# Kernel optimization log

Measured on AMD Instinct MI355X. Metric: run time of the kernel, lower is better.

Reference implementation:

```python
import jax, jax.numpy as jnp
import numpy as np

B, S, D, H = 8, 1024, 1024, 16
DK = D // H  # 64


def setup_inputs() -> dict:
    key = jax.random.key(0)
    k1, k2, k3, k4, k5, k6 = jax.random.split(key, 6)
    mask = jax.random.randint(k1, (B, S, S), 0, 2, dtype=jnp.int32)
    x_key_value = jax.random.normal(k2, (B, S, D), dtype=jnp.float32)
    # per-head projection weights (stacked over heads)
    scale = 1.0 / np.sqrt(D)
    wq = jax.random.normal(k3, (H, D, DK), dtype=jnp.float32) * scale
    wk = jax.random.normal(k4, (H, D, DK), dtype=jnp.float32) * scale
    wv = jax.random.normal(k5, (H, D, DK), dtype=jnp.float32) * scale
    # output projection (nn.Parameter; randomized here for a meaningful baseline)
    wo = jax.random.normal(k6, (D, D), dtype=jnp.float32) * scale
    return {"mask": mask, "x_key_value": x_key_value, "wq": wq, "wk": wk, "wv": wv, "wo": wo}


def reference(mask, x_key_value, wq, wk, wv, wo):
    # batched multi-head SDPA (equivalent to the per-head Python loop + concat)
    q = jnp.einsum('bsd,hdk->bhsk', x_key_value, wq)
    k = jnp.einsum('btd,hdk->bhtk', x_key_value, wk)
    v = jnp.einsum('btd,hdk->bhtk', x_key_value, wv)
    scores = jnp.einsum('bhsk,bhtk->bhst', q, k) / jnp.sqrt(jnp.asarray(DK, q.dtype))
    scores = jnp.where(mask[:, None, :, :] != 0, scores, jnp.asarray(-1e9, q.dtype))
    attn = jax.nn.softmax(scores, axis=-1)
    ctx = jnp.einsum('bhst,bhtk->bhsk', attn, v)
    # concat heads along feature dim: [B,S,H*DK]
    ctx = ctx.transpose(0, 2, 1, 3).reshape(B, S, D)
    # output proj (dropout is identity in eval) + residual
    res = ctx @ wo + x_key_value
    # torch.layer_norm over normalized_shape = (S, D), no affine, eps=1e-5
    mean = jnp.mean(res, axis=(1, 2), keepdims=True)
    var = jnp.var(res, axis=(1, 2), keepdims=True)
    return (res - mean) / jnp.sqrt(var + 1e-5)
```

## Files before the change

### kernel.cpp

```cpp
#include <hip/hip_runtime.h>

typedef unsigned short u16;
typedef __attribute__((ext_vector_type(8))) short bf16x8;
typedef __attribute__((ext_vector_type(4))) float f32x4;


static __device__ __forceinline__ u16 f2bf(float f) {
    union { float f; unsigned u; } v; v.f = f;
    unsigned r = v.u + 0x7fffu + ((v.u >> 16) & 1u);
    return (u16)(r >> 16);
}

static __device__ __forceinline__ f32x4 mfma16(bf16x8 a, bf16x8 b, f32x4 c) {
    return __builtin_amdgcn_mfma_f32_16x16x32_bf16(a, b, c, 0, 0, 0);
}

static __device__ __forceinline__ void load_lds16(const u16* g, u16* l) {
    __builtin_amdgcn_global_load_lds((const __attribute__((address_space(1))) unsigned*)(const void*)g,
                                     (__attribute__((address_space(3))) unsigned*)(void*)l, 16, 0, 0);
}

__global__ __launch_bounds__(256) void cvt_x_kernel(const float* __restrict__ x, u16* __restrict__ xb) {
    int i = (blockIdx.x * 256 + threadIdx.x) * 4;
    float4 v = *(const float4*)(x + i);
    ushort4 o;
    o.x = f2bf(v.x); o.y = f2bf(v.y); o.z = f2bf(v.z); o.w = f2bf(v.w);
    *(ushort4*)(xb + i) = o;
}

__global__ __launch_bounds__(256) void cvt_w_kernel(const float* __restrict__ wq, const float* __restrict__ wk,
                                                    const float* __restrict__ wv, const float* __restrict__ wo,
                                                    u16* __restrict__ wt, u16* __restrict__ wot) {
    int o = blockIdx.x * 256 + threadIdx.x;
    if (o < 3145728) {
        int z = o >> 20;
        int rem = o & 1048575;
        int n = rem >> 10;
        int d = rem & 1023;
        int h = n >> 6, kk = n & 63;
        const float* w = (z == 0) ? wq : (z == 1) ? wk : wv;
        wt[o] = f2bf(w[h * 65536 + d * 64 + kk]);
    } else {
        int oo = o - 3145728;
        int n = oo >> 10, d = oo & 1023;
        wot[oo] = f2bf(wo[d * 1024 + n]);
    }
}

__global__ __launch_bounds__(256) void pack_mask_kernel(const int* __restrict__ mask, uint2* __restrict__ mb) {
    long long wi = (long long)blockIdx.x * 4 + (threadIdx.x >> 6);
    int lane = threadIdx.x & 63;
    int v = mask[wi * 64 + lane];
    unsigned long long bal = __ballot(v != 0);
    if (lane == 0) {
        uint2 o; o.x = (unsigned)bal; o.y = (unsigned)(bal >> 32);
        mb[wi] = o;
    }
}

__global__ __launch_bounds__(256) void qkv_gemm_kernel(const u16* __restrict__ xb, const u16* __restrict__ wt,
                                                       u16* __restrict__ qb, u16* __restrict__ kb,
                                                       u16* __restrict__ vtb) {
    __shared__ __align__(16) u16 As[128 * 64];
    __shared__ __align__(16) u16 Bs[128 * 64];

    int t = threadIdx.x;
    int lane = t & 63, w = t >> 6;
    int wm = w & 1, wn = w >> 1;
    int l16 = lane & 15, quad = lane >> 4;
    int sw = l16 & 7;

    int m0 = blockIdx.x * 128;
    int n0g = blockIdx.y * 128;

    int srow = t >> 3;
    int skp = ((t & 7) ^ (srow & 7)) * 8;
    const u16* ga0 = xb + (m0 + srow) * 1024 + skp;
    const u16* gb0 = wt + (n0g + srow) * 1024 + skp;

    int arow0 = wm * 64 + l16;
    int brow0 = wn * 64 + l16;

    f32x4 acc[4][4];
#pragma unroll
    for (int i = 0; i < 4; ++i)
#pragma unroll
        for (int j = 0; j < 4; ++j) acc[i][j] = (f32x4){0.f, 0.f, 0.f, 0.f};

    for (int kb0 = 0; kb0 < 1024; kb0 += 64) {
        __syncthreads();
#pragma unroll
        for (int c = 0; c < 4; ++c)
            load_lds16(ga0 + c * 32768 + kb0, &As[c * 2048 + t * 8]);
#pragma unroll
        for (int c = 0; c < 4; ++c)
            load_lds16(gb0 + c * 32768 + kb0, &Bs[c * 2048 + t * 8]);
        __syncthreads();

#pragma unroll
        for (int kh = 0; kh < 2; ++kh) {
            int kidx = ((kh << 2) + quad) ^ sw;
            bf16x8 af[4], bfr[4];
#pragma unroll
            for (int i = 0; i < 4; ++i)
                af[i] = *(const bf16x8*)&As[(arow0 + i * 16) * 64 + kidx * 8];
#pragma unroll
            for (int j = 0; j < 4; ++j)
                bfr[j] = *(const bf16x8*)&Bs[(brow0 + j * 16) * 64 + kidx * 8];
#pragma unroll
            for (int i = 0; i < 4; ++i)
#pragma unroll
                for (int j = 0; j < 4; ++j)
                    acc[i][j] = mfma16(af[i], bfr[j], acc[i][j]);
        }
    }

    int z = blockIdx.y >> 3;
    float qscale = (z == 0) ? 0.125f : 1.0f;
#pragma unroll
    for (int j = 0; j < 4; ++j) {
        int ng = n0g + wn * 64 + j * 16 + l16;
        int nl = ng & 1023;
        int h = nl >> 6, kk = nl & 63;
#pragma unroll
        for (int i = 0; i < 4; ++i) {
#pragma unroll
            for (int r = 0; r < 4; ++r) {
                int m = m0 + wm * 64 + i * 16 + quad * 4 + r;
                int b_ = m >> 10, s = m & 1023;
                u16 val = f2bf(acc[i][j][r] * qscale);
                if (z == 0)      qb[((b_ * 16 + h) * 1024 + s) * 64 + kk] = val;
                else if (z == 1) kb[((b_ * 16 + h) * 1024 + s) * 64 + kk] = val;
                else             vtb[((b_ * 16 + h) * 64 + kk) * 1024 + s] = val;
            }
        }
    }
}

__global__ __launch_bounds__(256) void attn_kernel(const u16* __restrict__ qb, const u16* __restrict__ kb,
                                                   const u16* __restrict__ vtb, const uint2* __restrict__ mb,
                                                   u16* __restrict__ ctx) {
    __shared__ __align__(16) u16 Ks[64 * 64];
    __shared__ __align__(16) u16 Vs[64 * 64];
    __shared__ __align__(16) u16 P[4][16][72];

    int t = threadIdx.x;
    int w = t >> 6, lane = t & 63;
    int l16 = lane & 15, quad = lane >> 4;
    int h = blockIdx.y, b = blockIdx.z;
    int q0 = blockIdx.x * 64 + w * 16;

    const u16* Q = qb + (b * 16 + h) * 65536;
    const u16* K = kb + (b * 16 + h) * 65536;
    const u16* Vt = vtb + (b * 16 + h) * 65536;
    const uint2* MB = mb + (b * 1024 + q0) * 16;

    int srow = t >> 3;
    int skp = ((t & 7) ^ (srow & 7)) * 8;
    const u16* gk0 = K + srow * 64 + skp;
    const u16* gv0 = Vt + srow * 1024 + skp;

    bf16x8 qf0 = *(const bf16x8*)(Q + (q0 + l16) * 64 + quad * 8);
    bf16x8 qf1 = *(const bf16x8*)(Q + (q0 + l16) * 64 + 32 + quad * 8);

    f32x4 O[4];
#pragma unroll
    for (int j = 0; j < 4; ++j) O[j] = (f32x4){0.f, 0.f, 0.f, 0.f};
    float lsum[4] = {0.f, 0.f, 0.f, 0.f};

    int sw = l16 & 7;

    for (int kt0 = 0; kt0 < 16; ++kt0) {
        int k0 = kt0 * 64;
        __syncthreads();
#pragma unroll
        for (int c = 0; c < 2; ++c) {
            load_lds16(gk0 + (k0 + c * 32) * 64, &Ks[c * 2048 + t * 8]);
            load_lds16(gv0 + c * 32 * 1024 + k0, &Vs[c * 2048 + t * 8]);
        }
        __syncthreads();

        f32x4 s[4];
#pragma unroll
        for (int kt = 0; kt < 4; ++kt) {
            int row = kt * 16 + l16;
            bf16x8 klo = *(const bf16x8*)&Ks[row * 64 + ((quad ^ sw) * 8)];
            bf16x8 khi = *(const bf16x8*)&Ks[row * 64 + (((4 + quad) ^ sw) * 8)];
            f32x4 z = {0.f, 0.f, 0.f, 0.f};
            z = mfma16(qf0, klo, z);
            z = mfma16(qf1, khi, z);
            s[kt] = z;
        }

#pragma unroll
        for (int r = 0; r < 4; ++r) {
            int qrow = quad * 4 + r;
            uint2 mw = MB[qrow * 16 + kt0];
#pragma unroll
            for (int kt = 0; kt < 4; ++kt) {
                unsigned wsel = (kt < 2) ? mw.x : mw.y;
                unsigned bit = (wsel >> ((kt & 1) * 16 + l16)) & 1u;
                float e = bit ? __expf(s[kt][r]) : 0.f;
                lsum[r] += e;
                P[w][qrow][kt * 16 + l16] = f2bf(e);
            }
        }

        bf16x8 pf0 = *(const bf16x8*)&P[w][l16][quad * 8];
        bf16x8 pf1 = *(const bf16x8*)&P[w][l16][32 + quad * 8];

#pragma unroll
        for (int j = 0; j < 4; ++j) {
            int row = j * 16 + l16;
            bf16x8 vlo = *(const bf16x8*)&Vs[row * 64 + ((quad ^ sw) * 8)];
            bf16x8 vhi = *(const bf16x8*)&Vs[row * 64 + (((4 + quad) ^ sw) * 8)];
            O[j] = mfma16(pf0, vlo, O[j]);
            O[j] = mfma16(pf1, vhi, O[j]);
        }
    }

#pragma unroll
    for (int r = 0; r < 4; ++r) {
        float s = lsum[r];
        s += __shfl_xor(s, 1);
        s += __shfl_xor(s, 2);
        s += __shfl_xor(s, 4);
        s += __shfl_xor(s, 8);
        lsum[r] = s;
    }

#pragma unroll
    for (int r = 0; r < 4; ++r) {
        int sI = q0 + quad * 4 + r;
        float inv = 1.0f / lsum[r];
        int base = (b * 1024 + sI) * 1024 + h * 64;
#pragma unroll
        for (int j = 0; j < 4; ++j)
            ctx[base + j * 16 + l16] = f2bf(O[j][r] * inv);
    }
}

__global__ __launch_bounds__(256) void oproj_gemm_kernel(const u16* __restrict__ ctxb, const u16* __restrict__ wot,
                                                         const float* __restrict__ x, float* __restrict__ res) {
    __shared__ __align__(16) u16 As[128 * 64];
    __shared__ __align__(16) u16 Bs[128 * 64];

    int t = threadIdx.x;
    int lane = t & 63, w = t >> 6;
    int wm = w & 1, wn = w >> 1;
    int l16 = lane & 15, quad = lane >> 4;
    int sw = l16 & 7;

    int m0 = blockIdx.x * 128;
    int n0 = blockIdx.y * 128;

    int srow = t >> 3;
    int skp = ((t & 7) ^ (srow & 7)) * 8;
    const u16* ga0 = ctxb + (m0 + srow) * 1024 + skp;
    const u16* gb0 = wot + (n0 + srow) * 1024 + skp;

    int arow0 = wm * 64 + l16;
    int brow0 = wn * 64 + l16;

    f32x4 acc[4][4];
#pragma unroll
    for (int i = 0; i < 4; ++i)
#pragma unroll
        for (int j = 0; j < 4; ++j) acc[i][j] = (f32x4){0.f, 0.f, 0.f, 0.f};

    for (int kb0 = 0; kb0 < 1024; kb0 += 64) {
        __syncthreads();
#pragma unroll
        for (int c = 0; c < 4; ++c)
            load_lds16(ga0 + c * 32768 + kb0, &As[c * 2048 + t * 8]);
#pragma unroll
        for (int c = 0; c < 4; ++c)
            load_lds16(gb0 + c * 32768 + kb0, &Bs[c * 2048 + t * 8]);
        __syncthreads();

#pragma unroll
        for (int kh = 0; kh < 2; ++kh) {
            int kidx = ((kh << 2) + quad) ^ sw;
            bf16x8 af[4], bfr[4];
#pragma unroll
            for (int i = 0; i < 4; ++i)
                af[i] = *(const bf16x8*)&As[(arow0 + i * 16) * 64 + kidx * 8];
#pragma unroll
            for (int j = 0; j < 4; ++j)
                bfr[j] = *(const bf16x8*)&Bs[(brow0 + j * 16) * 64 + kidx * 8];
#pragma unroll
            for (int i = 0; i < 4; ++i)
#pragma unroll
                for (int j = 0; j < 4; ++j)
                    acc[i][j] = mfma16(af[i], bfr[j], acc[i][j]);
        }
    }

#pragma unroll
    for (int i = 0; i < 4; ++i) {
#pragma unroll
        for (int r = 0; r < 4; ++r) {
            int m = m0 + wm * 64 + i * 16 + quad * 4 + r;
#pragma unroll
            for (int j = 0; j < 4; ++j) {
                int n = n0 + wn * 64 + j * 16 + l16;
                res[m * 1024 + n] = acc[i][j][r] + x[m * 1024 + n];
            }
        }
    }
}

__global__ __launch_bounds__(256) void reduce_kernel(const float* __restrict__ res, float* __restrict__ sums) {
    int b = blockIdx.y;
    const float* p = res + b * 1048576;
    float s = 0.f, s2 = 0.f;
    for (int i = blockIdx.x * 256 + threadIdx.x; i < 1048576; i += 16384) {
        float v = p[i];
        s += v; s2 += v * v;
    }
#pragma unroll
    for (int off = 32; off > 0; off >>= 1) {
        s += __shfl_down(s, off);
        s2 += __shfl_down(s2, off);
    }
    __shared__ float ls[4], ls2[4];
    int w = threadIdx.x >> 6, lane = threadIdx.x & 63;
    if (lane == 0) { ls[w] = s; ls2[w] = s2; }
    __syncthreads();
    if (threadIdx.x == 0) {
        atomicAdd(&sums[b * 2 + 0], ls[0] + ls[1] + ls[2] + ls[3]);
        atomicAdd(&sums[b * 2 + 1], ls2[0] + ls2[1] + ls2[2] + ls2[3]);
    }
}

__global__ __launch_bounds__(256) void norm_kernel(const float* __restrict__ res, const float* __restrict__ sums,
                                                   float* __restrict__ out) {
    int i = blockIdx.x * 256 + threadIdx.x;
    int b = i >> 20;
    float mean = sums[b * 2 + 0] * (1.0f / 1048576.0f);
    float var = sums[b * 2 + 1] * (1.0f / 1048576.0f) - mean * mean;
    float rs = rsqrtf(var + 1e-5f);
    out[i] = (res[i] - mean) * rs;
}


extern "C" void kernel_launch(void* const* d_in, const int* in_sizes, int n_in,
                              void* d_out, int out_size, void* d_ws, size_t ws_size,
                              hipStream_t stream) {
    const int* mask  = (const int*)d_in[0];
    const float* x   = (const float*)d_in[1];
    const float* wq  = (const float*)d_in[2];
    const float* wk  = (const float*)d_in[3];
    const float* wv  = (const float*)d_in[4];
    const float* wo  = (const float*)d_in[5];
    float* out = (float*)d_out;

    char* ws = (char*)d_ws;
    u16* xb    = (u16*)(ws + 0);
    u16* wt    = (u16*)(ws + 16777216);
    u16* wot   = (u16*)(ws + 23068672);
    u16* qb    = (u16*)(ws + 25165824);
    u16* kb    = (u16*)(ws + 41943040);
    u16* vtb   = (u16*)(ws + 58720256);
    float* res = (float*)(ws + 25165824);
    float* sums = (float*)(ws + 75497472);
    uint2* mbits = (uint2*)(ws + 76546048);
    u16* ctxb  = (u16*)d_out;

    hipMemsetAsync(sums, 0, 64, stream);
    pack_mask_kernel<<<32768, 256, 0, stream>>>(mask, mbits);
    cvt_x_kernel<<<8192, 256, 0, stream>>>(x, xb);
    cvt_w_kernel<<<16384, 256, 0, stream>>>(wq, wk, wv, wo, wt, wot);
    qkv_gemm_kernel<<<dim3(64, 24), 256, 0, stream>>>(xb, wt, qb, kb, vtb);
    attn_kernel<<<dim3(16, 16, 8), 256, 0, stream>>>(qb, kb, vtb, mbits, ctxb);
    oproj_gemm_kernel<<<dim3(64, 8), 256, 0, stream>>>(ctxb, wot, x, res);
    reduce_kernel<<<dim3(64, 8), 256, 0, stream>>>(res, sums);
    norm_kernel<<<32768, 256, 0, stream>>>(res, sums, out);
}
```

Measured before the change: 361.9 us.

## Merge prep kernels, fuse LayerNorm stats into o-proj epilogue, prefetch mask words

The three preprocessing kernels (x conversion, weight transpose-convert, mask bit-packing) are merged into one launch that dispatches on block index. The separate reduction kernel is removed: the output-projection epilogue now accumulates per-block sum and sum-of-squares and atomically adds them per batch, which avoids re-reading the full residual tensor. In the attention loop the mask words are loaded before the barrier so their latency overlaps the K/V tile loads. The cost is more atomics per batch and extra register pressure in the GEMM epilogue.

```diff
diff --git a/kernel.cpp b/kernel.cpp
--- a/kernel.cpp
+++ b/kernel.cpp
@@ -20,41 +20,43 @@
                                      (__attribute__((address_space(3))) unsigned*)(void*)l, 16, 0, 0);
 }
 
-__global__ __launch_bounds__(256) void cvt_x_kernel(const float* __restrict__ x, u16* __restrict__ xb) {
-    int i = (blockIdx.x * 256 + threadIdx.x) * 4;
-    float4 v = *(const float4*)(x + i);
-    ushort4 o;
-    o.x = f2bf(v.x); o.y = f2bf(v.y); o.z = f2bf(v.z); o.w = f2bf(v.w);
-    *(ushort4*)(xb + i) = o;
-}
-
-__global__ __launch_bounds__(256) void cvt_w_kernel(const float* __restrict__ wq, const float* __restrict__ wk,
-                                                    const float* __restrict__ wv, const float* __restrict__ wo,
-                                                    u16* __restrict__ wt, u16* __restrict__ wot) {
-    int o = blockIdx.x * 256 + threadIdx.x;
-    if (o < 3145728) {
-        int z = o >> 20;
-        int rem = o & 1048575;
-        int n = rem >> 10;
-        int d = rem & 1023;
-        int h = n >> 6, kk = n & 63;
-        const float* w = (z == 0) ? wq : (z == 1) ? wk : wv;
-        wt[o] = f2bf(w[h * 65536 + d * 64 + kk]);
+__global__ __launch_bounds__(256) void prep_kernel(const float* __restrict__ x,
+                                                   const float* __restrict__ wq, const float* __restrict__ wk,
+                                                   const float* __restrict__ wv, const float* __restrict__ wo,
+                                                   const int* __restrict__ mask,
+                                                   u16* __restrict__ xb, u16* __restrict__ wt,
+                                                   u16* __restrict__ wot, uint2* __restrict__ mb) {
+    int bid = blockIdx.x;
+    if (bid < 8192) {
+        int i = (bid * 256 + threadIdx.x) * 4;
+        float4 v = *(const float4*)(x + i);
+        ushort4 o;
+        o.x = f2bf(v.x); o.y = f2bf(v.y); o.z = f2bf(v.z); o.w = f2bf(v.w);
+        *(ushort4*)(xb + i) = o;
+    } else if (bid < 24576) {
+        int o = (bid - 8192) * 256 + threadIdx.x;
+        if (o < 3145728) {
+            int z = o >> 20;
+            int rem = o & 1048575;
+            int n = rem >> 10;
+            int d = rem & 1023;
+            int h = n >> 6, kk = n & 63;
+            const float* w = (z == 0) ? wq : (z == 1) ? wk : wv;
+            wt[o] = f2bf(w[h * 65536 + d * 64 + kk]);
+        } else {
+            int oo = o - 3145728;
+            int n = oo >> 10, d = oo & 1023;
+            wot[oo] = f2bf(wo[d * 1024 + n]);
+        }
     } else {
-        int oo = o - 3145728;
-        int n = oo >> 10, d = oo & 1023;
-        wot[oo] = f2bf(wo[d * 1024 + n]);
-    }
-}
-
-__global__ __launch_bounds__(256) void pack_mask_kernel(const int* __restrict__ mask, uint2* __restrict__ mb) {
-    long long wi = (long long)blockIdx.x * 4 + (threadIdx.x >> 6);
-    int lane = threadIdx.x & 63;
-    int v = mask[wi * 64 + lane];
-    unsigned long long bal = __ballot(v != 0);
-    if (lane == 0) {
-        uint2 o; o.x = (unsigned)bal; o.y = (unsigned)(bal >> 32);
-        mb[wi] = o;
+        long long wi = (long long)(bid - 24576) * 4 + (threadIdx.x >> 6);
+        int lane = threadIdx.x & 63;
+        int v = mask[wi * 64 + lane];
+        unsigned long long bal = __ballot(v != 0);
+        if (lane == 0) {
+            uint2 o; o.x = (unsigned)bal; o.y = (unsigned)(bal >> 32);
+            mb[wi] = o;
+        }
     }
 }
 
@@ -172,6 +174,12 @@
 
     for (int kt0 = 0; kt0 < 16; ++kt0) {
         int k0 = kt0 * 64;
+
+        uint2 mw[4];
+#pragma unroll
+        for (int r = 0; r < 4; ++r)
+            mw[r] = MB[(quad * 4 + r) * 16 + kt0];
+
         __syncthreads();
 #pragma unroll
         for (int c = 0; c < 2; ++c) {
@@ -195,10 +203,9 @@
 #pragma unroll
         for (int r = 0; r < 4; ++r) {
             int qrow = quad * 4 + r;
-            uint2 mw = MB[qrow * 16 + kt0];
 #pragma unroll
             for (int kt = 0; kt < 4; ++kt) {
-                unsigned wsel = (kt < 2) ? mw.x : mw.y;
+                unsigned wsel = (kt < 2) ? mw[r].x : mw[r].y;
                 unsigned bit = (wsel >> ((kt & 1) * 16 + l16)) & 1u;
                 float e = bit ? __expf(s[kt][r]) : 0.f;
                 lsum[r] += e;
@@ -241,7 +248,8 @@
 }
 
 __global__ __launch_bounds__(256) void oproj_gemm_kernel(const u16* __restrict__ ctxb, const u16* __restrict__ wot,
-                                                         const float* __restrict__ x, float* __restrict__ res) {
+                                                         const float* __restrict__ x, float* __restrict__ res,
+                                                         float* __restrict__ sums) {
     __shared__ __align__(16) u16 As[128 * 64];
     __shared__ __align__(16) u16 Bs[128 * 64];
 
@@ -296,6 +304,7 @@
         }
     }
 
+    float ps = 0.f, ps2 = 0.f;
 #pragma unroll
     for (int i = 0; i < 4; ++i) {
 #pragma unroll
@@ -304,30 +313,23 @@
 #pragma unroll
             for (int j = 0; j < 4; ++j) {
                 int n = n0 + wn * 64 + j * 16 + l16;
-                res[m * 1024 + n] = acc[i][j][r] + x[m * 1024 + n];
+                float v = acc[i][j][r] + x[m * 1024 + n];
+                res[m * 1024 + n] = v;
+                ps += v; ps2 += v * v;
             }
         }
     }
-}
-
-__global__ __launch_bounds__(256) void reduce_kernel(const float* __restrict__ res, float* __restrict__ sums) {
-    int b = blockIdx.y;
-    const float* p = res + b * 1048576;
-    float s = 0.f, s2 = 0.f;
-    for (int i = blockIdx.x * 256 + threadIdx.x; i < 1048576; i += 16384) {
-        float v = p[i];
-        s += v; s2 += v * v;
-    }
+
 #pragma unroll
     for (int off = 32; off > 0; off >>= 1) {
-        s += __shfl_down(s, off);
-        s2 += __shfl_down(s2, off);
+        ps += __shfl_xor(ps, off);
+        ps2 += __shfl_xor(ps2, off);
     }
     __shared__ float ls[4], ls2[4];
-    int w = threadIdx.x >> 6, lane = threadIdx.x & 63;
-    if (lane == 0) { ls[w] = s; ls2[w] = s2; }
+    if (lane == 0) { ls[w] = ps; ls2[w] = ps2; }
     __syncthreads();
-    if (threadIdx.x == 0) {
+    if (t == 0) {
+        int b = blockIdx.x >> 3;
         atomicAdd(&sums[b * 2 + 0], ls[0] + ls[1] + ls[2] + ls[3]);
         atomicAdd(&sums[b * 2 + 1], ls2[0] + ls2[1] + ls2[2] + ls2[3]);
     }
@@ -368,12 +370,9 @@
     u16* ctxb  = (u16*)d_out;
 
     hipMemsetAsync(sums, 0, 64, stream);
-    pack_mask_kernel<<<32768, 256, 0, stream>>>(mask, mbits);
-    cvt_x_kernel<<<8192, 256, 0, stream>>>(x, xb);
-    cvt_w_kernel<<<16384, 256, 0, stream>>>(wq, wk, wv, wo, wt, wot);
+    prep_kernel<<<57344, 256, 0, stream>>>(x, wq, wk, wv, wo, mask, xb, wt, wot, mbits);
     qkv_gemm_kernel<<<dim3(64, 24), 256, 0, stream>>>(xb, wt, qb, kb, vtb);
     attn_kernel<<<dim3(16, 16, 8), 256, 0, stream>>>(qb, kb, vtb, mbits, ctxb);
-    oproj_gemm_kernel<<<dim3(64, 8), 256, 0, stream>>>(ctxb, wot, x, res);
-    reduce_kernel<<<dim3(64, 8), 256, 0, stream>>>(res, sums);
+    oproj_gemm_kernel<<<dim3(64, 8), 256, 0, stream>>>(ctxb, wot, x, res, sums);
     norm_kernel<<<32768, 256, 0, stream>>>(res, sums, out);
 }
```

After: 337.6 us. 1.07x faster.
